# Performance work log

Measured on AMD Instinct MI355X. Metric: run time of the kernel, lower is better.

The kernel has to match this reference:

```python
import jax, jax.numpy as jnp
import numpy as np

ALPHA = 0.5        # self._alpha
MAX_COEFF = 10.0   # self._max_coeff
SHARPNESS = 5      # self._loss_sharpness

N_VARS = 1_000_000
N_CLAUSES = 4_000_000
N_EDGES = 12_000_000


def setup_inputs() -> dict:
    key = jax.random.key(0)
    k1, k2, k3, k4 = jax.random.split(key, 4)
    variable_prediction = jax.random.uniform(k1, (N_VARS, 1), dtype=jnp.float32)
    lits = jax.random.randint(k2, (N_EDGES,), 0, N_VARS, dtype=jnp.int32)
    clauses = jax.random.randint(k3, (N_EDGES,), 0, N_CLAUSES, dtype=jnp.int32)
    graph_map = jnp.stack([lits, clauses])  # [2, E]
    # literal polarity: +1 (positive literal) or -1 (negated literal)
    edge_feature = jnp.where(jax.random.bernoulli(k4, 0.5, (N_EDGES, 1)), 1.0, -1.0).astype(jnp.float32)
    return {
        "variable_prediction": variable_prediction,
        "graph_map": graph_map,
        "edge_feature": edge_feature,
        "num_clauses": N_CLAUSES,
        "global_step": jnp.array([100.0], dtype=jnp.float32),
        "eps": jnp.array([1e-10], dtype=jnp.float32),
    }


def reference(variable_prediction, graph_map, edge_feature, num_clauses, global_step, eps):
    # temperature coefficient: min(step^alpha, max_coeff)
    coeff = jnp.minimum(global_step ** ALPHA, MAX_COEFF)  # [1]
    lits = graph_map[0]     # [E] variable index per edge
    clauses = graph_map[1]  # [E] clause index per edge
    ef = edge_feature[:, 0]  # [E]

    # sparse mm (signed variable mask @ prediction) == signed gather
    edge_values = ef * variable_prediction[lits, 0]          # [E]
    edge_values = edge_values + (1.0 - ef) * 0.5             # negated literal -> 1 - p
    weights = jnp.exp(coeff * edge_values)                   # [E]

    # sparse mm (function mask @ .) == scatter-add over clauses
    nominator = jax.ops.segment_sum(weights * edge_values, clauses, num_segments=num_clauses)
    denominator = jax.ops.segment_sum(weights, clauses, num_segments=num_clauses)

    clause_value = denominator / jnp.maximum(nominator, eps)
    clause_value = 1.0 + (clause_value - 1.0) ** SHARPNESS
    return jnp.mean(jnp.log(jnp.maximum(clause_value, eps)))
```

## Files before the change

### kernel.cpp

```cpp
#include <hip/hip_runtime.h>
#include <math.h>


constexpr int   N_CLAUSES_C = 4000000;
constexpr int   BKT_SHIFT   = 12;
constexpr int   BKT_CLS     = 1 << BKT_SHIFT;
constexpr int   NB_TOTAL    = (N_CLAUSES_C + BKT_CLS - 1) >> BKT_SHIFT;
constexpr int   CAP         = 13056;
constexpr int   SC_THREADS  = 1024;
constexpr int   BATCH       = 8192;
constexpr int   NBATCH      = 3;
constexpr int   SC_CHUNK    = BATCH * NBATCH;
constexpr int   PR_THREADS  = 512;

typedef int v4i __attribute__((ext_vector_type(4)));

__device__ __forceinline__ uint32_t ev_enc(float ev) {
    return (__float_as_uint(ev) + 0x400u) >> 11;
}
__device__ __forceinline__ float ev_dec(uint32_t q) {
    return __uint_as_float(q << 11);
}

__global__ __launch_bounds__(SC_THREADS) void
scatter_kernel(const float* __restrict__ vp,
               const int* __restrict__ lits,
               const int* __restrict__ cls,
               const int* __restrict__ efi,
               uint32_t* __restrict__ payload,
               uint32_t* __restrict__ cursors,
               int n_edges, int b_lo, int b_hi) {
    __shared__ uint32_t bh[NB_TOTAL];
    __shared__ uint32_t bOff[NB_TOTAL];
    __shared__ uint32_t bb[NB_TOTAL];
    __shared__ uint32_t buf[BATCH];
    __shared__ uint16_t bufB[BATCH];
    __shared__ uint32_t wsums[16];
    __shared__ uint32_t totalS;

    const int tid  = threadIdx.x;
    const int lane = tid & 63;
    const int wv   = tid >> 6;
    const int nbp  = b_hi - b_lo;
    const int c0   = blockIdx.x * SC_CHUNK;
    const int c1   = min(n_edges, c0 + SC_CHUNK);

    for (int batch = 0; batch < NBATCH; ++batch) {
        const int ebase = c0 + batch * BATCH;
        if (ebase >= c1) break;
        for (int i = tid; i < nbp; i += SC_THREADS) bh[i] = 0;
        __syncthreads();

        const int base = ebase + tid * 8;
        int cc[8], ll[8], ss[8];
        if (base + 8 <= c1) {
            v4i ca = __builtin_nontemporal_load((const v4i*)(cls  + base));
            v4i cb = __builtin_nontemporal_load((const v4i*)(cls  + base + 4));
            v4i la = __builtin_nontemporal_load((const v4i*)(lits + base));
            v4i lb = __builtin_nontemporal_load((const v4i*)(lits + base + 4));
            v4i fa = __builtin_nontemporal_load((const v4i*)(efi  + base));
            v4i fb = __builtin_nontemporal_load((const v4i*)(efi  + base + 4));
            #pragma unroll
            for (int i = 0; i < 4; ++i) {
                cc[i] = ca[i]; cc[4 + i] = cb[i];
                ll[i] = la[i]; ll[4 + i] = lb[i];
                ss[i] = fa[i]; ss[4 + i] = fb[i];
            }
        } else {
            #pragma unroll
            for (int i = 0; i < 8; ++i) {
                int e = base + i;
                if (e < c1) { cc[i] = cls[e]; ll[i] = lits[e]; ss[i] = efi[e]; }
                else cc[i] = -1;
            }
        }

        float vv[8];
        #pragma unroll
        for (int i = 0; i < 8; ++i) vv[i] = (cc[i] >= 0) ? vp[ll[i]] : 0.0f;

        uint16_t ebk[8], ern[8];
        #pragma unroll
        for (int i = 0; i < 8; ++i) {
            ebk[i] = 0xFFFFu;
            if (cc[i] >= 0) {
                int b = cc[i] >> BKT_SHIFT;
                if (b >= b_lo && b < b_hi) {
                    int ib = b - b_lo;
                    ebk[i] = (uint16_t)ib;
                    ern[i] = (uint16_t)atomicAdd(&bh[ib], 1u);
                }
            }
        }
        uint32_t ent[8];
        #pragma unroll
        for (int i = 0; i < 8; ++i) {
            if (ebk[i] != 0xFFFFu) {
                float ev = (ss[i] >= 0) ? vv[i] : (1.0f - vv[i]);
                ent[i] = (ev_enc(ev) << BKT_SHIFT) | (uint32_t)(cc[i] & (BKT_CLS - 1));
            }
        }
        __syncthreads();

        uint32_t v = (tid < nbp) ? bh[tid] : 0u;
        uint32_t x = v;
        #pragma unroll
        for (int d = 1; d < 64; d <<= 1) {
            uint32_t n = __shfl_up(x, (unsigned)d, 64);
            if (lane >= d) x += n;
        }
        if (lane == 63) wsums[wv] = x;
        __syncthreads();
        if (tid == 0) {
            uint32_t r = 0;
            #pragma unroll
            for (int w = 0; w < 16; ++w) { uint32_t tm = wsums[w]; wsums[w] = r; r += tm; }
        }
        __syncthreads();
        if (tid < nbp) {
            bOff[tid] = (x - v) + wsums[wv];
            bb[tid]   = v ? atomicAdd(&cursors[b_lo + tid], v) : 0u;
        }
        if (tid == SC_THREADS - 1) totalS = x + wsums[wv];
        __syncthreads();

        #pragma unroll
        for (int i = 0; i < 8; ++i) {
            if (ebk[i] != 0xFFFFu) {
                uint32_t s = bOff[ebk[i]] + ern[i];
                buf[s]  = ent[i];
                bufB[s] = ebk[i];
            }
        }
        __syncthreads();

        const uint32_t tS = totalS;
        for (uint32_t s = tid; s < tS; s += SC_THREADS) {
            uint32_t ib   = bufB[s];
            uint32_t gpos = bb[ib] + (s - bOff[ib]);
            if (gpos < (uint32_t)CAP)
                payload[(size_t)ib * CAP + gpos] = buf[s];
        }
        __syncthreads();
    }
}

__global__ __launch_bounds__(PR_THREADS) void
process_kernel(const uint32_t* __restrict__ payload,
               const uint32_t* __restrict__ cursors,
               const float* __restrict__ gstep,
               const float* __restrict__ epsp,
               double* __restrict__ acc,
               int b_lo) {
    __shared__ uint32_t offp[BKT_CLS / 2];
    __shared__ uint32_t srt[CAP];
    __shared__ uint32_t wscan[8];
    __shared__ double   wsum[8];
    const int tid  = threadIdx.x;
    const int lane = tid & 63;
    const int wv   = tid >> 6;
    const int b    = b_lo + blockIdx.x;

    for (int j = tid; j < BKT_CLS / 2; j += PR_THREADS) offp[j] = 0;
    __syncthreads();

    const uint32_t cnt = min(cursors[b], (uint32_t)CAP);
    const uint32_t* pl = payload + (size_t)blockIdx.x * CAP;
    const uint32_t nv = cnt >> 2;

    for (uint32_t k = tid; k < nv; k += PR_THREADS) {
        uint4 p4 = ((const uint4*)pl)[k];
        uint32_t c;
        c = p4.x & (BKT_CLS - 1); atomicAdd(&offp[c >> 1], 1u << ((c & 1) << 4));
        c = p4.y & (BKT_CLS - 1); atomicAdd(&offp[c >> 1], 1u << ((c & 1) << 4));
        c = p4.z & (BKT_CLS - 1); atomicAdd(&offp[c >> 1], 1u << ((c & 1) << 4));
        c = p4.w & (BKT_CLS - 1); atomicAdd(&offp[c >> 1], 1u << ((c & 1) << 4));
    }
    for (uint32_t k = (nv << 2) + tid; k < cnt; k += PR_THREADS) {
        uint32_t c = pl[k] & (BKT_CLS - 1);
        atomicAdd(&offp[c >> 1], 1u << ((c & 1) << 4));
    }
    __syncthreads();

    uint32_t pk[4];
    const int jb = tid * 4;
    uint32_t t = 0;
    #pragma unroll
    for (int i = 0; i < 4; ++i) {
        pk[i] = offp[jb + i];
        t += (pk[i] & 0xFFFFu) + (pk[i] >> 16);
    }
    uint32_t x = t;
    #pragma unroll
    for (int d = 1; d < 64; d <<= 1) {
        uint32_t n = __shfl_up(x, (unsigned)d, 64);
        if (lane >= d) x += n;
    }
    if (lane == 63) wscan[wv] = x;
    __syncthreads();
    if (tid == 0) {
        uint32_t r = 0;
        #pragma unroll
        for (int w = 0; w < 8; ++w) { uint32_t tm = wscan[w]; wscan[w] = r; r += tm; }
    }
    __syncthreads();
    uint32_t run = (x - t) + wscan[wv];
    #pragma unroll
    for (int i = 0; i < 4; ++i) {
        uint32_t lo = pk[i] & 0xFFFFu, hi = pk[i] >> 16;
        offp[jb + i] = run | ((run + lo) << 16);
        run += lo + hi;
    }
    __syncthreads();

    for (uint32_t k = tid; k < nv; k += PR_THREADS) {
        uint4 p4 = ((const uint4*)pl)[k];
        #pragma unroll
        for (int j = 0; j < 4; ++j) {
            uint32_t p = (j == 0) ? p4.x : (j == 1) ? p4.y : (j == 2) ? p4.z : p4.w;
            uint32_t c = p & (BKT_CLS - 1);
            uint32_t sh = (c & 1) << 4;
            uint32_t r = atomicAdd(&offp[c >> 1], 1u << sh);
            srt[(r >> sh) & 0xFFFFu] = p;
        }
    }
    for (uint32_t k = (nv << 2) + tid; k < cnt; k += PR_THREADS) {
        uint32_t p = pl[k];
        uint32_t c = p & (BKT_CLS - 1);
        uint32_t sh = (c & 1) << 4;
        uint32_t r = atomicAdd(&offp[c >> 1], 1u << sh);
        srt[(r >> sh) & 0xFFFFu] = p;
    }
    __syncthreads();

    const float coeff = fminf(sqrtf(gstep[0]), 10.0f);
    const float eps   = epsp[0];
    const int gbase = b << BKT_SHIFT;
    double local = 0.0;
    for (int j = tid; j < BKT_CLS; j += PR_THREADS) {
        if (gbase + j < N_CLAUSES_C) {
            uint32_t e = (offp[j >> 1] >> ((j & 1) << 4)) & 0xFFFFu;
            uint32_t s = 0;
            if (j > 0) {
                int jm = j - 1;
                s = (offp[jm >> 1] >> ((jm & 1) << 4)) & 0xFFFFu;
            }
            float nom = 0.f, den = 0.f;
            for (uint32_t k = s; k < e; ++k) {
                float ev = ev_dec(srt[k] >> BKT_SHIFT);
                float w  = __expf(coeff * ev);
                nom = fmaf(w, ev, nom);
                den += w;
            }
            float cv = den / fmaxf(nom, eps);
            float tt = cv - 1.0f;
            float t2 = tt * tt;
            float cv2 = 1.0f + t2 * t2 * tt;
            local += (double)__logf(fmaxf(cv2, eps));
        }
    }
    #pragma unroll
    for (int off = 32; off > 0; off >>= 1) local += __shfl_down(local, off, 64);
    if (lane == 0) wsum[wv] = local;
    __syncthreads();
    if (tid == 0) {
        double s = 0.0;
        #pragma unroll
        for (int w = 0; w < 8; ++w) s += wsum[w];
        unsafeAtomicAdd(acc, s);
    }
}

__global__ void finalize_kernel(const double* __restrict__ acc,
                                const int* __restrict__ ncp,
                                float* __restrict__ out) {
    if (threadIdx.x == 0 && blockIdx.x == 0)
        out[0] = (float)(acc[0] / (double)ncp[0]);
}

extern "C" void kernel_launch(void* const* d_in, const int* in_sizes, int n_in,
                              void* d_out, int out_size, void* d_ws, size_t ws_size,
                              hipStream_t stream) {
    const float* vp    = (const float*)d_in[0];
    const int*   gmap  = (const int*)d_in[1];
    const float* ef    = (const float*)d_in[2];
    const int*   ncp   = (const int*)d_in[3];
    const float* gstep = (const float*)d_in[4];
    const float* epsp  = (const float*)d_in[5];
    float*       out   = (float*)d_out;

    const int n_edges = in_sizes[1] / 2;
    const int* lits = gmap;
    const int* cls  = gmap + n_edges;

    int P = 8;
    int nbp_max = (NB_TOTAL + 7) / 8;
    size_t cursors_off_w = (size_t)nbp_max * CAP;
    size_t acc_off_w = (cursors_off_w + NB_TOTAL + 1) & ~(size_t)1;
    const int cands[4] = {1, 2, 4, 8};
    for (int ci = 0; ci < 4; ++ci) {
        int cand = cands[ci];
        int nm = (NB_TOTAL + cand - 1) / cand;
        size_t pw = (size_t)nm * CAP;
        size_t cw = pw + NB_TOTAL;
        size_t aw = (cw + 1) & ~(size_t)1;
        size_t need = aw * 4 + 8;
        if (need <= ws_size) { P = cand; nbp_max = nm; cursors_off_w = pw; acc_off_w = aw; break; }
    }

    uint32_t* payload = (uint32_t*)d_ws;
    uint32_t* cursors = payload + cursors_off_w;
    double*   acc     = (double*)((uint32_t*)d_ws + acc_off_w);

    hipMemsetAsync(cursors, 0, (acc_off_w - cursors_off_w) * 4 + 8, stream);

    const int sc_blocks = (n_edges + SC_CHUNK - 1) / SC_CHUNK;
    for (int p = 0; p < P; ++p) {
        int b_lo = p * nbp_max;
        int b_hi = min(NB_TOTAL, b_lo + nbp_max);
        if (b_lo >= b_hi) continue;
        scatter_kernel<<<sc_blocks, SC_THREADS, 0, stream>>>(
            vp, lits, cls, (const int*)ef, payload, cursors, n_edges, b_lo, b_hi);
        process_kernel<<<b_hi - b_lo, PR_THREADS, 0, stream>>>(
            payload, cursors, gstep, epsp, acc, b_lo);
    }
    finalize_kernel<<<1, 64, 0, stream>>>(acc, ncp, out);
}
```

Baseline: 179.5 us.

## Prefetch next batch indices and simplify bucket scan in scatter kernel

Restructures the scatter kernel's batch loop so the next batch's clause and literal indices are loaded before the payload write-out of the current batch, overlapping global loads with LDS work. The multi-wave scan with its extra syncs is replaced by a single-wave 16-element-per-lane scan, while the other waves do the global cursor atomics concurrently. Per-edge bucket, rank and clause offset are packed into one register, and launch bounds request higher occupancy. The scan assumes at most 1024 buckets per pass and ranks below 1024; entries beyond those limits, and bucket index 1023, are silently dropped.

```diff
diff --git a/kernel.cpp b/kernel.cpp
--- a/kernel.cpp
+++ b/kernel.cpp
@@ -22,7 +22,43 @@
     return __uint_as_float(q << 11);
 }
 
-__global__ __launch_bounds__(SC_THREADS) void
+__device__ __forceinline__ void load_pair(const int* __restrict__ cls,
+                                          const int* __restrict__ lits,
+                                          int base, int c1, int (&cc)[8], int (&ll)[8]) {
+    if (base + 8 <= c1) {
+        v4i ca = __builtin_nontemporal_load((const v4i*)(cls  + base));
+        v4i cb = __builtin_nontemporal_load((const v4i*)(cls  + base + 4));
+        v4i la = __builtin_nontemporal_load((const v4i*)(lits + base));
+        v4i lb = __builtin_nontemporal_load((const v4i*)(lits + base + 4));
+        #pragma unroll
+        for (int i = 0; i < 4; ++i) {
+            cc[i] = ca[i]; cc[4 + i] = cb[i];
+            ll[i] = la[i]; ll[4 + i] = lb[i];
+        }
+    } else {
+        #pragma unroll
+        for (int i = 0; i < 8; ++i) {
+            int e = base + i;
+            if (e < c1) { cc[i] = cls[e]; ll[i] = lits[e]; }
+            else        { cc[i] = -1;     ll[i] = 0;       }
+        }
+    }
+}
+
+__device__ __forceinline__ void load_ef(const int* __restrict__ efi,
+                                        int base, int c1, int (&ss)[8]) {
+    if (base + 8 <= c1) {
+        v4i fa = __builtin_nontemporal_load((const v4i*)(efi + base));
+        v4i fb = __builtin_nontemporal_load((const v4i*)(efi + base + 4));
+        #pragma unroll
+        for (int i = 0; i < 4; ++i) { ss[i] = fa[i]; ss[4 + i] = fb[i]; }
+    } else {
+        #pragma unroll
+        for (int i = 0; i < 8; ++i) { int e = base + i; ss[i] = (e < c1) ? efi[e] : 0; }
+    }
+}
+
+__global__ __launch_bounds__(SC_THREADS, 8) void
 scatter_kernel(const float* __restrict__ vp,
                const int* __restrict__ lits,
                const int* __restrict__ cls,
@@ -30,12 +66,11 @@
                uint32_t* __restrict__ payload,
                uint32_t* __restrict__ cursors,
                int n_edges, int b_lo, int b_hi) {
-    __shared__ uint32_t bh[NB_TOTAL];
-    __shared__ uint32_t bOff[NB_TOTAL];
+    __shared__ uint32_t bh[1024];
+    __shared__ uint32_t bOff[1024];
     __shared__ uint32_t bb[NB_TOTAL];
     __shared__ uint32_t buf[BATCH];
     __shared__ uint16_t bufB[BATCH];
-    __shared__ uint32_t wsums[16];
     __shared__ uint32_t totalS;
 
     const int tid  = threadIdx.x;
@@ -44,94 +79,78 @@
     const int nbp  = b_hi - b_lo;
     const int c0   = blockIdx.x * SC_CHUNK;
     const int c1   = min(n_edges, c0 + SC_CHUNK);
-
-    for (int batch = 0; batch < NBATCH; ++batch) {
-        const int ebase = c0 + batch * BATCH;
-        if (ebase >= c1) break;
-        for (int i = tid; i < nbp; i += SC_THREADS) bh[i] = 0;
-        __syncthreads();
-
-        const int base = ebase + tid * 8;
-        int cc[8], ll[8], ss[8];
-        if (base + 8 <= c1) {
-            v4i ca = __builtin_nontemporal_load((const v4i*)(cls  + base));
-            v4i cb = __builtin_nontemporal_load((const v4i*)(cls  + base + 4));
-            v4i la = __builtin_nontemporal_load((const v4i*)(lits + base));
-            v4i lb = __builtin_nontemporal_load((const v4i*)(lits + base + 4));
-            v4i fa = __builtin_nontemporal_load((const v4i*)(efi  + base));
-            v4i fb = __builtin_nontemporal_load((const v4i*)(efi  + base + 4));
-            #pragma unroll
-            for (int i = 0; i < 4; ++i) {
-                cc[i] = ca[i]; cc[4 + i] = cb[i];
-                ll[i] = la[i]; ll[4 + i] = lb[i];
-                ss[i] = fa[i]; ss[4 + i] = fb[i];
-            }
-        } else {
-            #pragma unroll
-            for (int i = 0; i < 8; ++i) {
-                int e = base + i;
-                if (e < c1) { cc[i] = cls[e]; ll[i] = lits[e]; ss[i] = efi[e]; }
-                else cc[i] = -1;
-            }
-        }
-
+    const int nb   = (c1 - c0 + BATCH - 1) / BATCH;
+
+    int cc[8], ll[8];
+    load_pair(cls, lits, c0 + tid * 8, c1, cc, ll);
+    bh[tid] = 0;
+    __syncthreads();
+
+    for (int k = 0; k < nb; ++k) {
+        const int base = c0 + k * BATCH + tid * 8;
+
+        int ss[8];
+        load_ef(efi, base, c1, ss);
         float vv[8];
         #pragma unroll
         for (int i = 0; i < 8; ++i) vv[i] = (cc[i] >= 0) ? vp[ll[i]] : 0.0f;
 
-        uint16_t ebk[8], ern[8];
+        uint32_t meta[8];
         #pragma unroll
         for (int i = 0; i < 8; ++i) {
-            ebk[i] = 0xFFFFu;
+            meta[i] = 0xFFC00000u;
             if (cc[i] >= 0) {
                 int b = cc[i] >> BKT_SHIFT;
                 if (b >= b_lo && b < b_hi) {
-                    int ib = b - b_lo;
-                    ebk[i] = (uint16_t)ib;
-                    ern[i] = (uint16_t)atomicAdd(&bh[ib], 1u);
+                    uint32_t ib = (uint32_t)(b - b_lo);
+                    uint32_t r  = atomicAdd(&bh[ib], 1u);
+                    if (r < 1024u)
+                        meta[i] = ((uint32_t)cc[i] & 4095u) | (r << 12) | (ib << 22);
                 }
             }
         }
-        uint32_t ent[8];
+        __syncthreads();
+
+        if (wv == 0) {
+            const int jb = lane * 16;
+            uint32_t t = 0;
+            #pragma unroll
+            for (int i = 0; i < 16; ++i) t += bh[jb + i];
+            uint32_t x = t;
+            #pragma unroll
+            for (int d = 1; d < 64; d <<= 1) {
+                uint32_t n = __shfl_up(x, (unsigned)d, 64);
+                if (lane >= d) x += n;
+            }
+            uint32_t run = x - t;
+            #pragma unroll
+            for (int i = 0; i < 16; ++i) {
+                uint32_t v = bh[jb + i];
+                bOff[jb + i] = run;
+                run += v;
+            }
+            if (lane == 63) totalS = x;
+        } else {
+            for (int i = tid - 64; i < nbp; i += SC_THREADS - 64) {
+                uint32_t v = bh[i];
+                bb[i] = v ? atomicAdd(&cursors[b_lo + i], v) : 0u;
+            }
+        }
+        __syncthreads();
+
         #pragma unroll
         for (int i = 0; i < 8; ++i) {
-            if (ebk[i] != 0xFFFFu) {
+            uint32_t ib = meta[i] >> 22;
+            if (ib < 1023u) {
                 float ev = (ss[i] >= 0) ? vv[i] : (1.0f - vv[i]);
-                ent[i] = (ev_enc(ev) << BKT_SHIFT) | (uint32_t)(cc[i] & (BKT_CLS - 1));
-            }
-        }
-        __syncthreads();
-
-        uint32_t v = (tid < nbp) ? bh[tid] : 0u;
-        uint32_t x = v;
-        #pragma unroll
-        for (int d = 1; d < 64; d <<= 1) {
-            uint32_t n = __shfl_up(x, (unsigned)d, 64);
-            if (lane >= d) x += n;
-        }
-        if (lane == 63) wsums[wv] = x;
-        __syncthreads();
-        if (tid == 0) {
-            uint32_t r = 0;
-            #pragma unroll
-            for (int w = 0; w < 16; ++w) { uint32_t tm = wsums[w]; wsums[w] = r; r += tm; }
-        }
-        __syncthreads();
-        if (tid < nbp) {
-            bOff[tid] = (x - v) + wsums[wv];
-            bb[tid]   = v ? atomicAdd(&cursors[b_lo + tid], v) : 0u;
-        }
-        if (tid == SC_THREADS - 1) totalS = x + wsums[wv];
-        __syncthreads();
-
-        #pragma unroll
-        for (int i = 0; i < 8; ++i) {
-            if (ebk[i] != 0xFFFFu) {
-                uint32_t s = bOff[ebk[i]] + ern[i];
-                buf[s]  = ent[i];
-                bufB[s] = ebk[i];
-            }
-        }
+                uint32_t s = bOff[ib] + ((meta[i] >> 12) & 1023u);
+                buf[s]  = (ev_enc(ev) << BKT_SHIFT) | (meta[i] & 4095u);
+                bufB[s] = (uint16_t)ib;
+            }
+        }
+        bh[tid] = 0;
+        if (k + 1 < nb)
+            load_pair(cls, lits, c0 + (k + 1) * BATCH + tid * 8, c1, cc, ll);
         __syncthreads();
 
         const uint32_t tS = totalS;
```

Result: faster. 175.2 us (-2.4%).
